# Performance work log

Measured on AMD Instinct MI355X. Metric: run time of the kernel, lower is better.

The kernel has to match this reference:

```python
import jax, jax.numpy as jnp
import numpy as np
from jax import lax

B, H, W = 4096, 8, 8
DICT, SE, E, NZ = 64, 8, 256, 1024
C1, C2 = 64, 128
EPS = 1e-4


def setup_inputs() -> dict:
    key = jax.random.key(0)
    ks = jax.random.split(key, 32)
    d = {}
    d['s'] = jax.random.randint(ks[0], (B, H, W), 0, DICT)
    d['s_prime'] = jax.random.randint(ks[1], (B, H, W), 0, DICT)
    d['w_embed'] = jax.random.normal(ks[2], (DICT, SE), dtype=jnp.float32)
    i = 3
    for p in ('p1', 'p2', 'p3'):
        d[p + '_w1'] = jax.random.normal(ks[i], (C1, SE, 3, 3), dtype=jnp.float32) * 0.1; i += 1
        d[p + '_b1'] = jax.random.normal(ks[i], (C1,), dtype=jnp.float32) * 0.1; i += 1
        d[p + '_w2'] = jax.random.normal(ks[i], (C2, C1, 3, 3), dtype=jnp.float32) * 0.05; i += 1
        d[p + '_b2'] = jax.random.normal(ks[i], (C2,), dtype=jnp.float32) * 0.05; i += 1
        d[p + '_lw'] = jax.random.normal(ks[i], (E, C2 * H * W), dtype=jnp.float32) * 0.02; i += 1
        d[p + '_lb'] = jax.random.normal(ks[i], (E,), dtype=jnp.float32) * 0.02; i += 1
    d['z_vectors'] = jax.random.normal(ks[i], (NZ, E), dtype=jnp.float32)
    d['scale'] = jnp.ones((1,), dtype=jnp.float32)
    return d


def _conv(x, w, b):
    # x: [B,C,H,W], w: [O,I,3,3], padding=1 == SAME for k=3
    y = lax.conv_general_dilated(x, w, (1, 1), 'SAME',
                                 dimension_numbers=('NCHW', 'OIHW', 'NCHW'))
    return y + b[None, :, None, None]


def _phi(x, w1, b1, w2, b2, lw, lb):
    # run_modules(..., last_activation=True): relu after every conv
    x = jax.nn.relu(_conv(x, w1, b1))
    x = jax.nn.relu(_conv(x, w2, b2))
    x = x.reshape(x.shape[0], -1)  # [B, C2*H*W]
    return x @ lw.T + lb  # [B, E]


def _normalized(m, eps):
    return m / (jnp.sqrt(jnp.sum(m * m, axis=1, keepdims=True)) + eps)


def reference(s, s_prime, w_embed,
              p1_w1, p1_b1, p1_w2, p1_b2, p1_lw, p1_lb,
              p2_w1, p2_b1, p2_w2, p2_b2, p2_lw, p2_lb,
              p3_w1, p3_b1, p3_w2, p3_b2, p3_lw, p3_lb,
              z_vectors, scale):
    # nn.Embedding(max_norm=1): renorm rows with norm > 1 to unit norm
    wn = jnp.sqrt(jnp.sum(w_embed * w_embed, axis=1, keepdims=True))
    w = w_embed * jnp.minimum(1.0, 1.0 / jnp.maximum(wn, 1e-7))
    s_embed = jnp.transpose(w[s], (0, 3, 1, 2))        # [B,SE,H,W]
    sp_embed = jnp.transpose(w[s_prime], (0, 3, 1, 2))  # embed_conv is None -> identity

    s_int = _phi(s_embed, p1_w1, p1_b1, p1_w2, p1_b2, p1_lw, p1_lb)            # phi1
    diff_int = _phi(sp_embed - s_embed, p2_w1, p2_b1, p2_w2, p2_b2, p2_lw, p2_lb)  # phi2
    sp_out = _normalized(_phi(sp_embed, p3_w1, p3_b1, p3_w2, p3_b2, p3_lw, p3_lb), EPS)  # phi3

    # quantize: cdist (p=2) against codebook, argmax (farthest, as in source), gather
    x2 = jnp.sum(diff_int * diff_int, axis=1, keepdims=True)      # [B,1]
    z2 = jnp.sum(z_vectors * z_vectors, axis=1)[None, :]          # [1,NZ]
    dist = jnp.sqrt(jnp.maximum(x2 + z2 - 2.0 * (diff_int @ z_vectors.T), 0.0))  # [B,NZ]
    z_inds = jnp.argmax(dist, axis=1)                              # [B]
    z_matrix = z_vectors[z_inds]                                   # [B,E]

    s_out = _normalized(s_int + z_matrix, EPS)                     # fc (fc_sizes=None)
    gram = s_out @ sp_out.T                                        # [B,B]
    return jnp.exp(scale) * gram
```

## Files before the change

### kernel.cpp

```cpp
#include <hip/hip_runtime.h>
#include <hip/hip_bf16.h>
#include <math.h>

#define NB 4096
#define SE 8
#define ND 64
#define C1 64
#define C2 128
#define NE 256
#define NZ 1024
#define CHUNK 2048
#define KACT 8192
#define KSPLIT 8

#define W1M_N (3*12*64*8)
#define W2M_N (3*18*128*32)
#define ZT_N  (256*1024)
#define PREP_TOTAL (W1M_N + W2M_N + ZT_N)
#define LW_N (NE*KACT)

typedef __attribute__((ext_vector_type(8))) short bf16x8;
typedef __attribute__((ext_vector_type(4))) float f32x4;
typedef __attribute__((ext_vector_type(8))) unsigned short u16x8;
typedef __attribute__((ext_vector_type(4))) unsigned short u16x4;

static __device__ __forceinline__ unsigned short f2bf(float v) {
  __hip_bfloat16 h = __float2bfloat16(v);
  return __builtin_bit_cast(unsigned short, h);
}
static __device__ __forceinline__ float bf2f(unsigned short u) {
  return __bfloat162float(__builtin_bit_cast(__hip_bfloat16, u));
}

__global__ __launch_bounds__(256) void prep_kernel(
    const float* __restrict__ w1_0, const float* __restrict__ w1_1, const float* __restrict__ w1_2,
    const float* __restrict__ w2_0, const float* __restrict__ w2_1, const float* __restrict__ w2_2,
    const float* __restrict__ z,
    unsigned short* __restrict__ w1mh, unsigned short* __restrict__ w1ml,
    unsigned short* __restrict__ w2mh, unsigned short* __restrict__ w2ml,
    float* __restrict__ zT)
{
  int idx = blockIdx.x * 256 + threadIdx.x;
  if (idx < W1M_N) {
    int p = idx / 6144; int r = idx - p*6144;
    int j = r >> 9; int rem = r & 511; int o = rem >> 3; int c = rem & 7;
    const float* w1 = (p == 0) ? w1_0 : (p == 1) ? w1_1 : w1_2;
    float v = (j < 9) ? w1[o*72 + c*9 + j] : 0.f;
    unsigned short h = f2bf(v);
    w1mh[idx] = h;
    w1ml[idx] = f2bf(v - bf2f(h));
  } else if (idx < W1M_N + W2M_N) {
    int r0 = idx - W1M_N;
    int p = r0 / (128*576); int r = r0 - p*(128*576);
    int o = r / 576; int rem = r - o*576; int j = rem >> 6; int c = rem & 63;
    const float* w2 = (p == 0) ? w2_0 : (p == 1) ? w2_1 : w2_2;
    float v = w2[o*576 + c*9 + j];
    unsigned short h = f2bf(v);
    const int d = p*(128*576) + ((j << 1) + (c >> 5))*4096 + o*32 + (c & 31);
    w2mh[d] = h;
    w2ml[d] = f2bf(v - bf2f(h));
  } else if (idx < PREP_TOTAL) {
    int r = idx - (W1M_N + W2M_N);
    int e = r >> 10, n = r & 1023;
    zT[r] = z[n*256 + e];
  }
}

__global__ __launch_bounds__(256) void prep_lw_kernel(
    const float* __restrict__ lw, unsigned short* __restrict__ lwh,
    unsigned short* __restrict__ lwl, int do_lo)
{
  int idx = blockIdx.x * 256 + threadIdx.x;
  float v = lw[idx];
  unsigned short h = f2bf(v);
  lwh[idx] = h;
  if (do_lo) lwl[idx] = f2bf(v - bf2f(h));
}

template<int PASSES>
__global__ __launch_bounds__(256, 4) void conv_phi_kernel(
    const int* __restrict__ s, const int* __restrict__ sp,
    const float* __restrict__ w_embed,
    const unsigned short* __restrict__ w1mh, const unsigned short* __restrict__ w1ml,
    const float* __restrict__ b1,
    const unsigned short* __restrict__ w2mh, const unsigned short* __restrict__ w2ml,
    const float* __restrict__ b2,
    unsigned short* __restrict__ acth, unsigned short* __restrict__ actl,
    int mode, int b_start)
{
  __shared__ float wtab[ND][SE+1];
  __shared__ int sidx[64];
  __shared__ int spidx[64];
  __shared__ __align__(16) unsigned short xph[960];
  __shared__ __align__(16) unsigned short xpl[960];
  __shared__ __align__(16) unsigned short c1h[7680];
  __shared__ __align__(16) unsigned short c1l[7680];

  const int tid = threadIdx.x;
  const int b = b_start + blockIdx.x;

  {
    int4 z4 = {0,0,0,0};
    for (int t = tid; t < 120; t += 256) { ((int4*)xph)[t] = z4; ((int4*)xpl)[t] = z4; }
    for (int t = tid; t < 960; t += 256) { ((int4*)c1h)[t] = z4; ((int4*)c1l)[t] = z4; }
  }

  if (tid < 64) {
    sidx[tid] = s[b*64 + tid];
    float v[SE]; float ss = 0.f;
    #pragma unroll
    for (int c = 0; c < SE; ++c) { v[c] = w_embed[tid*SE + c]; ss += v[c]*v[c]; }
    float nrm = sqrtf(ss);
    float sc = fminf(1.f, 1.f / fmaxf(nrm, 1e-7f));
    #pragma unroll
    for (int c = 0; c < SE; ++c) wtab[tid][c] = v[c] * sc;
  } else if (tid < 128) {
    spidx[tid - 64] = sp[b*64 + tid - 64];
  }
  __syncthreads();

  if (tid < 64) {
    const int y = tid >> 3, x = tid & 7;
    const float* r0 = wtab[sidx[tid]];
    const float* r1 = wtab[spidx[tid]];
    u16x8 hv, lv;
    #pragma unroll
    for (int c = 0; c < SE; ++c) {
      float e0 = r0[c], e1 = r1[c];
      float v = (mode == 0) ? e0 : (mode == 1) ? (e1 - e0) : e1;
      unsigned short h = f2bf(v);
      hv[c] = h;
      lv[c] = f2bf(v - bf2f(h));
    }
    const int lin = (y + 1)*12 + (x + 1);
    *(u16x8*)(xph + lin*8) = hv;
    *(u16x8*)(xpl + lin*8) = lv;
  }
  __syncthreads();

  {
    const int lane = tid & 63, wid = tid >> 6;
    const int ph = wid;
    const int l15 = lane & 15, lk4 = lane >> 4;

    f32x4 a1[4];
    #pragma unroll
    for (int fm = 0; fm < 4; ++fm) a1[fm] = (f32x4){0.f,0.f,0.f,0.f};

    #pragma unroll
    for (int kk = 0; kk < 3; ++kk) {
      const int j = (kk << 2) + lk4;
      const int jc = (j > 8) ? 8 : j;
      const int dy = jc / 3, dx = jc - 3*(jc/3);
      bf16x8 Wh[4], Wl[4];
      #pragma unroll
      for (int fm = 0; fm < 4; ++fm) {
        const int o = (fm << 4) + l15;
        Wh[fm] = *(const bf16x8*)(w1mh + (j << 9) + (o << 3));
        Wl[fm] = *(const bf16x8*)(w1ml + (j << 9) + (o << 3));
      }
      const int p = (ph << 4) + l15;
      const int lin = ((p >> 3) + dy)*12 + (p & 7) + dx;
      const bf16x8 Xh = *(const bf16x8*)(xph + (lin << 3));
      const bf16x8 Xl = *(const bf16x8*)(xpl + (lin << 3));
      __builtin_amdgcn_s_setprio(1);
      #pragma unroll
      for (int fm = 0; fm < 4; ++fm) {
        a1[fm] = __builtin_amdgcn_mfma_f32_16x16x32_bf16(Wh[fm], Xh, a1[fm], 0, 0, 0);
        a1[fm] = __builtin_amdgcn_mfma_f32_16x16x32_bf16(Wl[fm], Xh, a1[fm], 0, 0, 0);
        a1[fm] = __builtin_amdgcn_mfma_f32_16x16x32_bf16(Wh[fm], Xl, a1[fm], 0, 0, 0);
      }
      __builtin_amdgcn_s_setprio(0);
    }

    const int p = (ph << 4) + l15;
    const int lin = ((p >> 3) + 1)*12 + (p & 7) + 1;
    #pragma unroll
    for (int fm = 0; fm < 4; ++fm) {
      const int obase = (fm << 4) + (lk4 << 2);
      const float4 bv = *(const float4*)(b1 + obase);
      const int idx2 = (obase >> 3)*960 + lin*8 + (obase & 7);
      u16x4 hv, lv;
      {
        float v0 = fmaxf(a1[fm][0] + bv.x, 0.f);
        float v1 = fmaxf(a1[fm][1] + bv.y, 0.f);
        float v2 = fmaxf(a1[fm][2] + bv.z, 0.f);
        float v3 = fmaxf(a1[fm][3] + bv.w, 0.f);
        hv[0] = f2bf(v0); hv[1] = f2bf(v1); hv[2] = f2bf(v2); hv[3] = f2bf(v3);
        lv[0] = f2bf(v0 - bf2f(hv[0])); lv[1] = f2bf(v1 - bf2f(hv[1]));
        lv[2] = f2bf(v2 - bf2f(hv[2])); lv[3] = f2bf(v3 - bf2f(hv[3]));
      }
      *(u16x4*)(c1h + idx2) = hv;
      *(u16x4*)(c1l + idx2) = lv;
    }
  }
  __syncthreads();

  {
    const int lane = tid & 63, wid = tid >> 6;
    const int ob = wid << 5;
    const int l15 = lane & 15, lk4 = lane >> 4;
    const int y0b = l15 >> 3, x0 = l15 & 7;

    f32x4 acc[4][2];
    #pragma unroll
    for (int mf = 0; mf < 4; ++mf)
      #pragma unroll
      for (int nf = 0; nf < 2; ++nf) acc[mf][nf] = (f32x4){0.f,0.f,0.f,0.f};

    #pragma unroll
    for (int j = 0; j < 9; ++j) {
      const int dy = j / 3, dx = j - 3*(j/3);
      #pragma unroll
      for (int h2 = 0; h2 < 2; ++h2) {
        const int sbase = ((j << 1) + h2) << 12;
        bf16x8 Bh[2], Bl[2];
        #pragma unroll
        for (int nf = 0; nf < 2; ++nf) {
          const int orow = ob + (nf << 4) + l15;
          const int a = sbase + orow*32 + (lk4 << 3);
          Bh[nf] = *(const bf16x8*)(w2mh + a);
          if (PASSES == 3) Bl[nf] = *(const bf16x8*)(w2ml + a);
        }
        const int cbk = (h2 << 2) + lk4;
        bf16x8 Ah[4], Al[4];
        #pragma unroll
        for (int mf = 0; mf < 4; ++mf) {
          const int lin = ((mf << 1) + y0b + dy)*12 + x0 + dx;
          const int a = cbk*960 + lin*8;
          Ah[mf] = *(const bf16x8*)(c1h + a);
          Al[mf] = *(const bf16x8*)(c1l + a);
        }
        __builtin_amdgcn_s_setprio(1);
        #pragma unroll
        for (int mf = 0; mf < 4; ++mf) {
          #pragma unroll
          for (int nf = 0; nf < 2; ++nf) {
            acc[mf][nf] = __builtin_amdgcn_mfma_f32_16x16x32_bf16(Ah[mf], Bh[nf], acc[mf][nf], 0, 0, 0);
            acc[mf][nf] = __builtin_amdgcn_mfma_f32_16x16x32_bf16(Al[mf], Bh[nf], acc[mf][nf], 0, 0, 0);
            if (PASSES == 3)
              acc[mf][nf] = __builtin_amdgcn_mfma_f32_16x16x32_bf16(Ah[mf], Bl[nf], acc[mf][nf], 0, 0, 0);
          }
        }
        __builtin_amdgcn_s_setprio(0);
      }
    }

    const size_t rowbase = (size_t)blockIdx.x * 8192;
    #pragma unroll
    for (int nf = 0; nf < 2; ++nf) {
      const int col = ob + (nf << 4) + l15;
      const float bv = b2[col];
      #pragma unroll
      for (int mf = 0; mf < 4; ++mf) {
        const int p0 = mf*16 + lk4*4;
        u16x4 hv, lv;
        #pragma unroll
        for (int r2 = 0; r2 < 4; ++r2) {
          float v = fmaxf(acc[mf][nf][r2] + bv, 0.f);
          unsigned short hq = f2bf(v);
          hv[r2] = hq;
          lv[r2] = f2bf(v - bf2f(hq));
        }
        *(u16x4*)(acth + rowbase + col*64 + p0) = hv;
        if (PASSES == 3)
          *(u16x4*)(actl + rowbase + col*64 + p0) = lv;
      }
    }
  }
}

template<int PASSES>
__global__ __launch_bounds__(256) void gemm_lds_tn(
    const unsigned short* __restrict__ Ahp, const unsigned short* __restrict__ Alp,
    const unsigned short* __restrict__ Bhp, const unsigned short* __restrict__ Blp,
    int K, float* __restrict__ Cdirect, float* __restrict__ Cpart,
    const float* __restrict__ bias, const float* __restrict__ scale_ptr)
{
  constexpr int NOP = (PASSES == 3) ? 2 : 1;
  __shared__ __align__(16) unsigned short As[NOP][128*64];
  __shared__ __align__(16) unsigned short Bs[NOP][64*64];

  const int tid = threadIdx.x;
  const int lane = tid & 63, wid = tid >> 6;
  const int wm = wid >> 1, wn = wid & 1;
  const int l15 = lane & 15, lk4 = lane >> 4;
  const int M = gridDim.x << 7, N = gridDim.y << 6;
  const int KC = K / gridDim.z;
  const int bm = blockIdx.x << 7, bn = blockIdx.y << 6;
  const int kbase = blockIdx.z * KC;
  const int NT = KC >> 6;

  const int sr = tid >> 3;
  const int sc8 = (tid & 7) * 8;

  const unsigned short* gA[NOP];
  const unsigned short* gB[NOP];
  gA[0] = Ahp; gB[0] = Bhp;
  if (PASSES == 3) { gA[1] = Alp; gB[1] = Blp; }

  u16x8 ra[NOP][4], rb[NOP][2];

  f32x4 acc[4][2];
  #pragma unroll
  for (int fm = 0; fm < 4; ++fm)
    #pragma unroll
    for (int nf = 0; nf < 2; ++nf) acc[fm][nf] = (f32x4){0.f,0.f,0.f,0.f};

  {
    const int k0 = kbase + sc8;
    #pragma unroll
    for (int p = 0; p < NOP; ++p) {
      #pragma unroll
      for (int i = 0; i < 4; ++i)
        ra[p][i] = *(const u16x8*)(gA[p] + (size_t)(bm + sr + i*32) * K + k0);
      #pragma unroll
      for (int i = 0; i < 2; ++i)
        rb[p][i] = *(const u16x8*)(gB[p] + (size_t)(bn + sr + i*32) * K + k0);
    }
  }

  for (int t = 0; t < NT; ++t) {
    __syncthreads();
    #pragma unroll
    for (int p = 0; p < NOP; ++p) {
      #pragma unroll
      for (int i = 0; i < 4; ++i) {
        const int r = sr + i*32;
        *(u16x8*)(&As[p][r*64 + (sc8 ^ ((r & 7) << 3))]) = ra[p][i];
      }
      #pragma unroll
      for (int i = 0; i < 2; ++i) {
        const int r = sr + i*32;
        *(u16x8*)(&Bs[p][r*64 + (sc8 ^ ((r & 7) << 3))]) = rb[p][i];
      }
    }
    __syncthreads();
    if (t + 1 < NT) {
      const int k0 = kbase + ((t + 1) << 6) + sc8;
      #pragma unroll
      for (int p = 0; p < NOP; ++p) {
        #pragma unroll
        for (int i = 0; i < 4; ++i)
          ra[p][i] = *(const u16x8*)(gA[p] + (size_t)(bm + sr + i*32) * K + k0);
        #pragma unroll
        for (int i = 0; i < 2; ++i)
          rb[p][i] = *(const u16x8*)(gB[p] + (size_t)(bn + sr + i*32) * K + k0);
      }
    }
    #pragma unroll
    for (int ks = 0; ks < 2; ++ks) {
      const int kb = ks*32 + lk4*8;
      bf16x8 af[NOP][4], bf[NOP][2];
      #pragma unroll
      for (int p = 0; p < NOP; ++p) {
        #pragma unroll
        for (int fm = 0; fm < 4; ++fm) {
          const int r = wm*64 + fm*16 + l15;
          af[p][fm] = *(const bf16x8*)(&As[p][r*64 + (kb ^ ((r & 7) << 3))]);
        }
        #pragma unroll
        for (int nf = 0; nf < 2; ++nf) {
          const int r = wn*32 + nf*16 + l15;
          bf[p][nf] = *(const bf16x8*)(&Bs[p][r*64 + (kb ^ ((r & 7) << 3))]);
        }
      }
      #pragma unroll
      for (int fm = 0; fm < 4; ++fm) {
        #pragma unroll
        for (int nf = 0; nf < 2; ++nf) {
          acc[fm][nf] = __builtin_amdgcn_mfma_f32_16x16x32_bf16(af[0][fm], bf[0][nf], acc[fm][nf], 0, 0, 0);
          if (PASSES == 3) {
            acc[fm][nf] = __builtin_amdgcn_mfma_f32_16x16x32_bf16(af[0][fm], bf[1][nf], acc[fm][nf], 0, 0, 0);
            acc[fm][nf] = __builtin_amdgcn_mfma_f32_16x16x32_bf16(af[1][fm], bf[0][nf], acc[fm][nf], 0, 0, 0);
          }
        }
      }
    }
  }

  if (Cpart) {
    float* base = Cpart + (size_t)blockIdx.z * ((size_t)M * N);
    #pragma unroll
    for (int fm = 0; fm < 4; ++fm) {
      #pragma unroll
      for (int nf = 0; nf < 2; ++nf) {
        const int row0 = bm + wm*64 + fm*16 + lk4*4;
        const int col  = bn + wn*32 + nf*16 + l15;
        #pragma unroll
        for (int r2 = 0; r2 < 4; ++r2)
          base[(size_t)(row0 + r2) * N + col] = acc[fm][nf][r2];
      }
    }
  } else {
    float alpha = scale_ptr ? expf(scale_ptr[0]) : 1.f;
    #pragma unroll
    for (int fm = 0; fm < 4; ++fm) {
      #pragma unroll
      for (int nf = 0; nf < 2; ++nf) {
        const int row0 = bm + wm*64 + fm*16 + lk4*4;
        const int col  = bn + wn*32 + nf*16 + l15;
        const float bv = bias ? bias[col] : 0.f;
        #pragma unroll
        for (int r2 = 0; r2 < 4; ++r2)
          Cdirect[(size_t)(row0 + r2) * N + col] = alpha * acc[fm][nf][r2] + bv;
      }
    }
  }
}

__global__ __launch_bounds__(256) void reduce_bias_kernel(
    const float* __restrict__ part, const float* __restrict__ bias, float* __restrict__ out)
{
  const int idx = blockIdx.x * 256 + threadIdx.x;
  float a = bias[idx & (NE-1)];
  #pragma unroll
  for (int q = 0; q < KSPLIT; ++q) a += part[(size_t)q * (CHUNK*NE) + idx];
  out[idx] = a;
}

__global__ __launch_bounds__(256) void quant_kernel(
    const float* __restrict__ diff, const float* __restrict__ zT, int* __restrict__ z_ind)
{
  __shared__ __align__(16) float d[8][NE];
  __shared__ float wv[8][4];
  __shared__ int wni[8][4];
  const int tid = threadIdx.x;
  const int b0 = blockIdx.x * 8;
  for (int j = tid; j < 8*NE; j += 256) (&d[0][0])[j] = diff[(size_t)b0*NE + j];
  __syncthreads();

  float zz[4] = {0.f, 0.f, 0.f, 0.f};
  float dot[8][4] = {};
  for (int e = 0; e < NE; e += 4) {
    float4 dd[8];
    #pragma unroll
    for (int r = 0; r < 8; ++r) dd[r] = *(const float4*)(&d[r][e]);
    #pragma unroll
    for (int u = 0; u < 4; ++u) {
      const float* zr = zT + (size_t)(e + u) * NZ + tid;
      float z0 = zr[0], z1 = zr[256], z2 = zr[512], z3 = zr[768];
      zz[0] = fmaf(z0, z0, zz[0]); zz[1] = fmaf(z1, z1, zz[1]);
      zz[2] = fmaf(z2, z2, zz[2]); zz[3] = fmaf(z3, z3, zz[3]);
      #pragma unroll
      for (int r = 0; r < 8; ++r) {
        const float de = (u == 0) ? dd[r].x : (u == 1) ? dd[r].y : (u == 2) ? dd[r].z : dd[r].w;
        dot[r][0] = fmaf(z0, de, dot[r][0]);
        dot[r][1] = fmaf(z1, de, dot[r][1]);
        dot[r][2] = fmaf(z2, de, dot[r][2]);
        dot[r][3] = fmaf(z3, de, dot[r][3]);
      }
    }
  }

  const int lane = tid & 63, wid = tid >> 6;
  #pragma unroll
  for (int r = 0; r < 8; ++r) {
    float best = zz[0] - 2.f*dot[r][0]; int bi = tid;
    float v1 = zz[1] - 2.f*dot[r][1]; if (v1 > best) { best = v1; bi = tid + 256; }
    float v2 = zz[2] - 2.f*dot[r][2]; if (v2 > best) { best = v2; bi = tid + 512; }
    float v3 = zz[3] - 2.f*dot[r][3]; if (v3 > best) { best = v3; bi = tid + 768; }
    for (int m = 1; m < 64; m <<= 1) {
      float ov = __shfl_xor(best, m, 64);
      int   oi = __shfl_xor(bi, m, 64);
      if (ov > best || (ov == best && oi < bi)) { best = ov; bi = oi; }
    }
    if (lane == 0) { wv[r][wid] = best; wni[r][wid] = bi; }
  }
  __syncthreads();
  if (tid < 8) {
    float best = wv[tid][0]; int bi = wni[tid][0];
    #pragma unroll
    for (int w = 1; w < 4; ++w) {
      float v = wv[tid][w]; int n = wni[tid][w];
      if (v > best || (v == best && n < bi)) { best = v; bi = n; }
    }
    z_ind[b0 + tid] = bi;
  }
}

__global__ __launch_bounds__(256) void norm_to_bf16_kernel(
    const float* __restrict__ v, unsigned short* __restrict__ ob)
{
  const int row = blockIdx.x*4 + (threadIdx.x >> 6);
  const int lane = threadIdx.x & 63;
  float4 x = ((const float4*)v)[(size_t)row*64 + lane];
  float ss = x.x*x.x + x.y*x.y + x.z*x.z + x.w*x.w;
  #pragma unroll
  for (int m = 1; m < 64; m <<= 1) ss += __shfl_xor(ss, m, 64);
  float sc = 1.f / (sqrtf(ss) + 1e-4f);
  u16x4 o;
  o[0] = f2bf(x.x*sc); o[1] = f2bf(x.y*sc); o[2] = f2bf(x.z*sc); o[3] = f2bf(x.w*sc);
  *(u16x4*)(ob + (size_t)row*NE + lane*4) = o;
}

__global__ __launch_bounds__(256) void build_sout_kernel(
    const float* __restrict__ s_int, const float* __restrict__ z,
    const int* __restrict__ z_ind, unsigned short* __restrict__ ob)
{
  const int row = blockIdx.x*4 + (threadIdx.x >> 6);
  const int lane = threadIdx.x & 63;
  const int zi = z_ind[row];
  float4 a = *((const float4*)s_int + (size_t)row*64 + lane);
  float4 c = *((const float4*)z + (size_t)zi*64 + lane);
  float4 x = {a.x + c.x, a.y + c.y, a.z + c.z, a.w + c.w};
  float ss = x.x*x.x + x.y*x.y + x.z*x.z + x.w*x.w;
  #pragma unroll
  for (int m = 1; m < 64; m <<= 1) ss += __shfl_xor(ss, m, 64);
  float sc = 1.f / (sqrtf(ss) + 1e-4f);
  u16x4 o;
  o[0] = f2bf(x.x*sc); o[1] = f2bf(x.y*sc); o[2] = f2bf(x.z*sc); o[3] = f2bf(x.w*sc);
  *(u16x4*)(ob + (size_t)row*NE + lane*4) = o;
}

extern "C" void kernel_launch(void* const* d_in, const int* in_sizes, int n_in,
                              void* d_out, int out_size, void* d_ws, size_t ws_size,
                              hipStream_t stream)
{
  const int* s  = (const int*)d_in[0];
  const int* sp = (const int*)d_in[1];
  const float* w_embed = (const float*)d_in[2];
  const float* z = (const float*)d_in[21];
  const float* scale = (const float*)d_in[22];
  float* out = (float*)d_out;

  size_t off = 0;
  auto allocB = [&](size_t bytes) -> void* {
    void* p = (void*)((char*)d_ws + off);
    off += ((bytes + 255) & ~(size_t)255);
    return p;
  };
  unsigned short* w1mh  = (unsigned short*)allocB((size_t)W1M_N * 2);
  unsigned short* w1ml  = (unsigned short*)allocB((size_t)W1M_N * 2);
  unsigned short* w2mh  = (unsigned short*)allocB((size_t)W2M_N * 2);
  unsigned short* w2ml  = (unsigned short*)allocB((size_t)W2M_N * 2);
  float* zT             = (float*)allocB(ZT_N * 4);
  unsigned short* lwh   = (unsigned short*)allocB((size_t)LW_N * 2);
  unsigned short* lwl   = (unsigned short*)allocB((size_t)LW_N * 2);
  float* s_int          = (float*)allocB((size_t)NB * NE * 4);
  float* diff_int       = (float*)allocB((size_t)NB * NE * 4);
  float* sp_out         = (float*)allocB((size_t)NB * NE * 4);
  unsigned short* soutb = (unsigned short*)allocB((size_t)NB * NE * 2);
  unsigned short* spoutb= (unsigned short*)allocB((size_t)NB * NE * 2);
  int*   z_ind          = (int*)allocB(NB * 4);
  float* part           = (float*)allocB((size_t)CHUNK * NE * KSPLIT * 4);

  unsigned short* acth = (unsigned short*)d_out;
  unsigned short* actl = acth + (size_t)CHUNK * KACT;

  prep_kernel<<<PREP_TOTAL/256, 256, 0, stream>>>(
      (const float*)d_in[3],  (const float*)d_in[9],  (const float*)d_in[15],
      (const float*)d_in[5],  (const float*)d_in[11], (const float*)d_in[17],
      z, w1mh, w1ml, w2mh, w2ml, zT);

  for (int phi = 0; phi < 3; ++phi) {
    const float* b1 = (const float*)d_in[4 + phi*6];
    const float* b2 = (const float*)d_in[6 + phi*6];
    const float* lw = (const float*)d_in[7 + phi*6];
    const float* lb = (const float*)d_in[8 + phi*6];
    float* outvec = (phi == 0) ? s_int : (phi == 1) ? diff_int : sp_out;

    prep_lw_kernel<<<LW_N/256, 256, 0, stream>>>(lw, lwh, lwl, phi == 1);

    for (int b0 = 0; b0 < NB; b0 += CHUNK) {
      if (phi == 1)
        conv_phi_kernel<3><<<CHUNK, 256, 0, stream>>>(
            s, sp, w_embed, w1mh + phi*6144, w1ml + phi*6144, b1,
            w2mh + phi*(128*576), w2ml + phi*(128*576), b2,
            acth, actl, phi, b0);
      else
        conv_phi_kernel<2><<<CHUNK, 256, 0, stream>>>(
            s, sp, w_embed, w1mh + phi*6144, w1ml + phi*6144, b1,
            w2mh + phi*(128*576), w2ml + phi*(128*576), b2,
            acth, actl, phi, b0);
      dim3 g(CHUNK/128, NE/64, KSPLIT);
      if (phi == 1)
        gemm_lds_tn<3><<<g, 256, 0, stream>>>(acth, actl, lwh, lwl,
            KACT, nullptr, part, nullptr, nullptr);
      else
        gemm_lds_tn<1><<<g, 256, 0, stream>>>(acth, nullptr, lwh, nullptr,
            KACT, nullptr, part, nullptr, nullptr);
      reduce_bias_kernel<<<(CHUNK*NE)/256, 256, 0, stream>>>(part, lb, outvec + (size_t)b0*NE);
    }
  }

  norm_to_bf16_kernel<<<NB/4, 256, 0, stream>>>(sp_out, spoutb);
  quant_kernel<<<NB/8, 256, 0, stream>>>(diff_int, zT, z_ind);
  build_sout_kernel<<<NB/4, 256, 0, stream>>>(s_int, z, z_ind, soutb);

  dim3 gg(NB/128, NB/64, 1);
  gemm_lds_tn<1><<<gg, 256, 0, stream>>>(soutb, nullptr, spoutb, nullptr,
      NE, out, nullptr, nullptr, scale);
}
```

Baseline: 531.4 us.

## Switch conv2 to 32x32x16 MFMA tiles and precompute normalized embedding table

Measured after the change: 561.3 us. 5.6% more time.

```diff
diff --git a/kernel.cpp b/kernel.cpp
--- a/kernel.cpp
+++ b/kernel.cpp
@@ -14,13 +14,15 @@
 #define KSPLIT 8
 
 #define W1M_N (3*12*64*8)
-#define W2M_N (3*18*128*32)
+#define W2M_N (3*36*128*16)
 #define ZT_N  (256*1024)
 #define PREP_TOTAL (W1M_N + W2M_N + ZT_N)
+#define PREP_TOTAL2 (PREP_TOTAL + 512)
 #define LW_N (NE*KACT)
 
 typedef __attribute__((ext_vector_type(8))) short bf16x8;
 typedef __attribute__((ext_vector_type(4))) float f32x4;
+typedef __attribute__((ext_vector_type(16))) float f32x16;
 typedef __attribute__((ext_vector_type(8))) unsigned short u16x8;
 typedef __attribute__((ext_vector_type(4))) unsigned short u16x4;
 
@@ -35,10 +37,10 @@
 __global__ __launch_bounds__(256) void prep_kernel(
     const float* __restrict__ w1_0, const float* __restrict__ w1_1, const float* __restrict__ w1_2,
     const float* __restrict__ w2_0, const float* __restrict__ w2_1, const float* __restrict__ w2_2,
-    const float* __restrict__ z,
+    const float* __restrict__ z, const float* __restrict__ w_embed,
     unsigned short* __restrict__ w1mh, unsigned short* __restrict__ w1ml,
     unsigned short* __restrict__ w2mh, unsigned short* __restrict__ w2ml,
-    float* __restrict__ zT)
+    float* __restrict__ zT, float* __restrict__ wnorm)
 {
   int idx = blockIdx.x * 256 + threadIdx.x;
   if (idx < W1M_N) {
@@ -52,17 +54,28 @@
   } else if (idx < W1M_N + W2M_N) {
     int r0 = idx - W1M_N;
     int p = r0 / (128*576); int r = r0 - p*(128*576);
-    int o = r / 576; int rem = r - o*576; int j = rem >> 6; int c = rem & 63;
+    int slice = r >> 11; int rem = r & 2047;
+    int och = rem >> 4; int k = rem & 15;
+    int j = slice >> 2, q = slice & 3;
+    int c = (q << 4) + k;
     const float* w2 = (p == 0) ? w2_0 : (p == 1) ? w2_1 : w2_2;
-    float v = w2[o*576 + c*9 + j];
+    float v = w2[och*576 + c*9 + j];
     unsigned short h = f2bf(v);
-    const int d = p*(128*576) + ((j << 1) + (c >> 5))*4096 + o*32 + (c & 31);
-    w2mh[d] = h;
-    w2ml[d] = f2bf(v - bf2f(h));
+    w2mh[r0] = h;
+    w2ml[r0] = f2bf(v - bf2f(h));
   } else if (idx < PREP_TOTAL) {
     int r = idx - (W1M_N + W2M_N);
     int e = r >> 10, n = r & 1023;
     zT[r] = z[n*256 + e];
+  } else if (idx < PREP_TOTAL2) {
+    int t = idx - PREP_TOTAL;
+    int o = t >> 3, c = t & 7;
+    float ss = 0.f;
+    #pragma unroll
+    for (int e = 0; e < 8; ++e) { float u = w_embed[o*8 + e]; ss += u*u; }
+    float nrm = sqrtf(ss);
+    float sc = fminf(1.f, 1.f / fmaxf(nrm, 1e-7f));
+    wnorm[o*8 + c] = w_embed[o*8 + c] * sc;
   }
 }
 
@@ -80,7 +93,7 @@
 template<int PASSES>
 __global__ __launch_bounds__(256, 4) void conv_phi_kernel(
     const int* __restrict__ s, const int* __restrict__ sp,
-    const float* __restrict__ w_embed,
+    const float* __restrict__ wnorm,
     const unsigned short* __restrict__ w1mh, const unsigned short* __restrict__ w1ml,
     const float* __restrict__ b1,
     const unsigned short* __restrict__ w2mh, const unsigned short* __restrict__ w2ml,
@@ -88,9 +101,6 @@
     unsigned short* __restrict__ acth, unsigned short* __restrict__ actl,
     int mode, int b_start)
 {
-  __shared__ float wtab[ND][SE+1];
-  __shared__ int sidx[64];
-  __shared__ int spidx[64];
   __shared__ __align__(16) unsigned short xph[960];
   __shared__ __align__(16) unsigned short xpl[960];
   __shared__ __align__(16) unsigned short c1h[7680];
@@ -104,35 +114,26 @@
     for (int t = tid; t < 120; t += 256) { ((int4*)xph)[t] = z4; ((int4*)xpl)[t] = z4; }
     for (int t = tid; t < 960; t += 256) { ((int4*)c1h)[t] = z4; ((int4*)c1l)[t] = z4; }
   }
+  __syncthreads();
 
   if (tid < 64) {
-    sidx[tid] = s[b*64 + tid];
-    float v[SE]; float ss = 0.f;
-    #pragma unroll
-    for (int c = 0; c < SE; ++c) { v[c] = w_embed[tid*SE + c]; ss += v[c]*v[c]; }
-    float nrm = sqrtf(ss);
-    float sc = fminf(1.f, 1.f / fmaxf(nrm, 1e-7f));
-    #pragma unroll
-    for (int c = 0; c < SE; ++c) wtab[tid][c] = v[c] * sc;
-  } else if (tid < 128) {
-    spidx[tid - 64] = sp[b*64 + tid - 64];
-  }
-  __syncthreads();
-
-  if (tid < 64) {
-    const int y = tid >> 3, x = tid & 7;
-    const float* r0 = wtab[sidx[tid]];
-    const float* r1 = wtab[spidx[tid]];
+    const int si  = s[b*64 + tid];
+    const int spi = sp[b*64 + tid];
+    const float4 a0 = *(const float4*)(wnorm + si*8);
+    const float4 a1v = *(const float4*)(wnorm + si*8 + 4);
+    const float4 c0 = *(const float4*)(wnorm + spi*8);
+    const float4 c1v = *(const float4*)(wnorm + spi*8 + 4);
+    float e0[8] = {a0.x,a0.y,a0.z,a0.w, a1v.x,a1v.y,a1v.z,a1v.w};
+    float e1[8] = {c0.x,c0.y,c0.z,c0.w, c1v.x,c1v.y,c1v.z,c1v.w};
     u16x8 hv, lv;
     #pragma unroll
     for (int c = 0; c < SE; ++c) {
-      float e0 = r0[c], e1 = r1[c];
-      float v = (mode == 0) ? e0 : (mode == 1) ? (e1 - e0) : e1;
+      float v = (mode == 0) ? e0[c] : (mode == 1) ? (e1[c] - e0[c]) : e1[c];
       unsigned short h = f2bf(v);
       hv[c] = h;
       lv[c] = f2bf(v - bf2f(h));
     }
-    const int lin = (y + 1)*12 + (x + 1);
+    const int lin = ((tid >> 3) + 1)*12 + (tid & 7) + 1;
     *(u16x8*)(xph + lin*8) = hv;
     *(u16x8*)(xpl + lin*8) = lv;
   }
@@ -198,49 +199,44 @@
 
   {
     const int lane = tid & 63, wid = tid >> 6;
-    const int ob = wid << 5;
-    const int l15 = lane & 15, lk4 = lane >> 4;
-    const int y0b = l15 >> 3, x0 = l15 & 7;
-
-    f32x4 acc[4][2];
-    #pragma unroll
-    for (int mf = 0; mf < 4; ++mf)
-      #pragma unroll
-      for (int nf = 0; nf < 2; ++nf) acc[mf][nf] = (f32x4){0.f,0.f,0.f,0.f};
+    const int mt = wid >> 1;
+    const int np = wid & 1;
+    const int l31 = lane & 31, lh = lane >> 5;
+    const int p = (mt << 5) + l31;
+    const int py = p >> 3, px = p & 7;
+
+    f32x16 acc[2];
+    #pragma unroll
+    for (int nt = 0; nt < 2; ++nt)
+      #pragma unroll
+      for (int e = 0; e < 16; ++e) acc[nt][e] = 0.f;
 
     #pragma unroll
     for (int j = 0; j < 9; ++j) {
       const int dy = j / 3, dx = j - 3*(j/3);
-      #pragma unroll
-      for (int h2 = 0; h2 < 2; ++h2) {
-        const int sbase = ((j << 1) + h2) << 12;
+      const int lin = (py + dy)*12 + px + dx;
+      #pragma unroll
+      for (int q = 0; q < 4; ++q) {
+        const int slice = (j << 2) + q;
+        const int cb = (q << 1) + lh;
+        const int aofs = cb*960 + (lin << 3);
+        const bf16x8 Ah = *(const bf16x8*)(c1h + aofs);
+        const bf16x8 Al = *(const bf16x8*)(c1l + aofs);
         bf16x8 Bh[2], Bl[2];
         #pragma unroll
-        for (int nf = 0; nf < 2; ++nf) {
-          const int orow = ob + (nf << 4) + l15;
-          const int a = sbase + orow*32 + (lk4 << 3);
-          Bh[nf] = *(const bf16x8*)(w2mh + a);
-          if (PASSES == 3) Bl[nf] = *(const bf16x8*)(w2ml + a);
-        }
-        const int cbk = (h2 << 2) + lk4;
-        bf16x8 Ah[4], Al[4];
-        #pragma unroll
-        for (int mf = 0; mf < 4; ++mf) {
-          const int lin = ((mf << 1) + y0b + dy)*12 + x0 + dx;
-          const int a = cbk*960 + lin*8;
-          Ah[mf] = *(const bf16x8*)(c1h + a);
-          Al[mf] = *(const bf16x8*)(c1l + a);
+        for (int nt = 0; nt < 2; ++nt) {
+          const int och = (np << 6) + (nt << 5) + l31;
+          const int bofs = (slice << 11) + (och << 4) + (lh << 3);
+          Bh[nt] = *(const bf16x8*)(w2mh + bofs);
+          if (PASSES == 3) Bl[nt] = *(const bf16x8*)(w2ml + bofs);
         }
         __builtin_amdgcn_s_setprio(1);
         #pragma unroll
-        for (int mf = 0; mf < 4; ++mf) {
-          #pragma unroll
-          for (int nf = 0; nf < 2; ++nf) {
-            acc[mf][nf] = __builtin_amdgcn_mfma_f32_16x16x32_bf16(Ah[mf], Bh[nf], acc[mf][nf], 0, 0, 0);
-            acc[mf][nf] = __builtin_amdgcn_mfma_f32_16x16x32_bf16(Al[mf], Bh[nf], acc[mf][nf], 0, 0, 0);
-            if (PASSES == 3)
-              acc[mf][nf] = __builtin_amdgcn_mfma_f32_16x16x32_bf16(Ah[mf], Bl[nf], acc[mf][nf], 0, 0, 0);
-          }
+        for (int nt = 0; nt < 2; ++nt) {
+          acc[nt] = __builtin_amdgcn_mfma_f32_32x32x16_bf16(Ah, Bh[nt], acc[nt], 0, 0, 0);
+          acc[nt] = __builtin_amdgcn_mfma_f32_32x32x16_bf16(Al, Bh[nt], acc[nt], 0, 0, 0);
+          if (PASSES == 3)
+            acc[nt] = __builtin_amdgcn_mfma_f32_32x32x16_bf16(Ah, Bl[nt], acc[nt], 0, 0, 0);
         }
         __builtin_amdgcn_s_setprio(0);
       }
@@ -248,23 +244,23 @@
 
     const size_t rowbase = (size_t)blockIdx.x * 8192;
     #pragma unroll
-    for (int nf = 0; nf < 2; ++nf) {
-      const int col = ob + (nf << 4) + l15;
+    for (int nt = 0; nt < 2; ++nt) {
+      const int col = (np << 6) + (nt << 5) + l31;
       const float bv = b2[col];
       #pragma unroll
-      for (int mf = 0; mf < 4; ++mf) {
-        const int p0 = mf*16 + lk4*4;
+      for (int rq = 0; rq < 4; ++rq) {
+        const int prow = (mt << 5) + (rq << 3) + (lh << 2);
         u16x4 hv, lv;
         #pragma unroll
-        for (int r2 = 0; r2 < 4; ++r2) {
-          float v = fmaxf(acc[mf][nf][r2] + bv, 0.f);
+        for (int rr = 0; rr < 4; ++rr) {
+          float v = fmaxf(acc[nt][(rq << 2) + rr] + bv, 0.f);
           unsigned short hq = f2bf(v);
-          hv[r2] = hq;
-          lv[r2] = f2bf(v - bf2f(hq));
+          hv[rr] = hq;
+          lv[rr] = f2bf(v - bf2f(hq));
         }
-        *(u16x4*)(acth + rowbase + col*64 + p0) = hv;
+        *(u16x4*)(acth + rowbase + col*64 + prow) = hv;
         if (PASSES == 3)
-          *(u16x4*)(actl + rowbase + col*64 + p0) = lv;
+          *(u16x4*)(actl + rowbase + col*64 + prow) = lv;
       }
     }
   }
@@ -535,6 +531,7 @@
   unsigned short* w2mh  = (unsigned short*)allocB((size_t)W2M_N * 2);
   unsigned short* w2ml  = (unsigned short*)allocB((size_t)W2M_N * 2);
   float* zT             = (float*)allocB(ZT_N * 4);
+  float* wnorm          = (float*)allocB(64 * 8 * 4);
   unsigned short* lwh   = (unsigned short*)allocB((size_t)LW_N * 2);
   unsigned short* lwl   = (unsigned short*)allocB((size_t)LW_N * 2);
   float* s_int          = (float*)allocB((size_t)NB * NE * 4);
@@ -548,10 +545,10 @@
   unsigned short* acth = (unsigned short*)d_out;
   unsigned short* actl = acth + (size_t)CHUNK * KACT;
 
-  prep_kernel<<<PREP_TOTAL/256, 256, 0, stream>>>(
+  prep_kernel<<<PREP_TOTAL2/256, 256, 0, stream>>>(
       (const float*)d_in[3],  (const float*)d_in[9],  (const float*)d_in[15],
       (const float*)d_in[5],  (const float*)d_in[11], (const float*)d_in[17],
-      z, w1mh, w1ml, w2mh, w2ml, zT);
+      z, w_embed, w1mh, w1ml, w2mh, w2ml, zT, wnorm);
 
   for (int phi = 0; phi < 3; ++phi) {
     const float* b1 = (const float*)d_in[4 + phi*6];
@@ -565,12 +562,12 @@
     for (int b0 = 0; b0 < NB; b0 += CHUNK) {
       if (phi == 1)
         conv_phi_kernel<3><<<CHUNK, 256, 0, stream>>>(
-            s, sp, w_embed, w1mh + phi*6144, w1ml + phi*6144, b1,
+            s, sp, wnorm, w1mh + phi*6144, w1ml + phi*6144, b1,
             w2mh + phi*(128*576), w2ml + phi*(128*576), b2,
             acth, actl, phi, b0);
       else
         conv_phi_kernel<2><<<CHUNK, 256, 0, stream>>>(
-            s, sp, w_embed, w1mh + phi*6144, w1ml + phi*6144, b1,
+            s, sp, wnorm, w1mh + phi*6144, w1ml + phi*6144, b1,
             w2mh + phi*(128*576), w2ml + phi*(128*576), b2,
             acth, actl, phi, b0);
       dim3 g(CHUNK/128, NE/64, KSPLIT);
```

## Precompute normalized embedding table and retile conv2 warp layout to 2x4 fragments

Applied to the files above, without the earlier changes.

Result: slower. 621.6 us (+17.0%).

```diff
diff --git a/kernel.cpp b/kernel.cpp
--- a/kernel.cpp
+++ b/kernel.cpp
@@ -17,6 +17,7 @@
 #define W2M_N (3*18*128*32)
 #define ZT_N  (256*1024)
 #define PREP_TOTAL (W1M_N + W2M_N + ZT_N)
+#define PREP_TOTAL2 (PREP_TOTAL + 512)
 #define LW_N (NE*KACT)
 
 typedef __attribute__((ext_vector_type(8))) short bf16x8;
@@ -35,10 +36,10 @@
 __global__ __launch_bounds__(256) void prep_kernel(
     const float* __restrict__ w1_0, const float* __restrict__ w1_1, const float* __restrict__ w1_2,
     const float* __restrict__ w2_0, const float* __restrict__ w2_1, const float* __restrict__ w2_2,
-    const float* __restrict__ z,
+    const float* __restrict__ z, const float* __restrict__ w_embed,
     unsigned short* __restrict__ w1mh, unsigned short* __restrict__ w1ml,
     unsigned short* __restrict__ w2mh, unsigned short* __restrict__ w2ml,
-    float* __restrict__ zT)
+    float* __restrict__ zT, float* __restrict__ wnorm)
 {
   int idx = blockIdx.x * 256 + threadIdx.x;
   if (idx < W1M_N) {
@@ -63,6 +64,15 @@
     int r = idx - (W1M_N + W2M_N);
     int e = r >> 10, n = r & 1023;
     zT[r] = z[n*256 + e];
+  } else if (idx < PREP_TOTAL2) {
+    int t = idx - PREP_TOTAL;
+    int o = t >> 3, c = t & 7;
+    float ss = 0.f;
+    #pragma unroll
+    for (int e = 0; e < 8; ++e) { float u = w_embed[o*8 + e]; ss += u*u; }
+    float nrm = sqrtf(ss);
+    float sc = fminf(1.f, 1.f / fmaxf(nrm, 1e-7f));
+    wnorm[o*8 + c] = w_embed[o*8 + c] * sc;
   }
 }
 
@@ -80,7 +90,7 @@
 template<int PASSES>
 __global__ __launch_bounds__(256, 4) void conv_phi_kernel(
     const int* __restrict__ s, const int* __restrict__ sp,
-    const float* __restrict__ w_embed,
+    const float* __restrict__ wnorm,
     const unsigned short* __restrict__ w1mh, const unsigned short* __restrict__ w1ml,
     const float* __restrict__ b1,
     const unsigned short* __restrict__ w2mh, const unsigned short* __restrict__ w2ml,
@@ -88,9 +98,6 @@
     unsigned short* __restrict__ acth, unsigned short* __restrict__ actl,
     int mode, int b_start)
 {
-  __shared__ float wtab[ND][SE+1];
-  __shared__ int sidx[64];
-  __shared__ int spidx[64];
   __shared__ __align__(16) unsigned short xph[960];
   __shared__ __align__(16) unsigned short xpl[960];
   __shared__ __align__(16) unsigned short c1h[7680];
@@ -104,35 +111,26 @@
     for (int t = tid; t < 120; t += 256) { ((int4*)xph)[t] = z4; ((int4*)xpl)[t] = z4; }
     for (int t = tid; t < 960; t += 256) { ((int4*)c1h)[t] = z4; ((int4*)c1l)[t] = z4; }
   }
+  __syncthreads();
 
   if (tid < 64) {
-    sidx[tid] = s[b*64 + tid];
-    float v[SE]; float ss = 0.f;
-    #pragma unroll
-    for (int c = 0; c < SE; ++c) { v[c] = w_embed[tid*SE + c]; ss += v[c]*v[c]; }
-    float nrm = sqrtf(ss);
-    float sc = fminf(1.f, 1.f / fmaxf(nrm, 1e-7f));
-    #pragma unroll
-    for (int c = 0; c < SE; ++c) wtab[tid][c] = v[c] * sc;
-  } else if (tid < 128) {
-    spidx[tid - 64] = sp[b*64 + tid - 64];
-  }
-  __syncthreads();
-
-  if (tid < 64) {
-    const int y = tid >> 3, x = tid & 7;
-    const float* r0 = wtab[sidx[tid]];
-    const float* r1 = wtab[spidx[tid]];
+    const int si  = s[b*64 + tid];
+    const int spi = sp[b*64 + tid];
+    const float4 a0 = *(const float4*)(wnorm + si*8);
+    const float4 a1v = *(const float4*)(wnorm + si*8 + 4);
+    const float4 c0 = *(const float4*)(wnorm + spi*8);
+    const float4 c1v = *(const float4*)(wnorm + spi*8 + 4);
+    float e0[8] = {a0.x,a0.y,a0.z,a0.w, a1v.x,a1v.y,a1v.z,a1v.w};
+    float e1[8] = {c0.x,c0.y,c0.z,c0.w, c1v.x,c1v.y,c1v.z,c1v.w};
     u16x8 hv, lv;
     #pragma unroll
     for (int c = 0; c < SE; ++c) {
-      float e0 = r0[c], e1 = r1[c];
-      float v = (mode == 0) ? e0 : (mode == 1) ? (e1 - e0) : e1;
+      float v = (mode == 0) ? e0[c] : (mode == 1) ? (e1[c] - e0[c]) : e1[c];
       unsigned short h = f2bf(v);
       hv[c] = h;
       lv[c] = f2bf(v - bf2f(h));
     }
-    const int lin = (y + 1)*12 + (x + 1);
+    const int lin = ((tid >> 3) + 1)*12 + (tid & 7) + 1;
     *(u16x8*)(xph + lin*8) = hv;
     *(u16x8*)(xpl + lin*8) = lv;
   }
@@ -198,15 +196,15 @@
 
   {
     const int lane = tid & 63, wid = tid >> 6;
-    const int ob = wid << 5;
+    const int mh = wid >> 1;
+    const int oh = wid & 1;
     const int l15 = lane & 15, lk4 = lane >> 4;
-    const int y0b = l15 >> 3, x0 = l15 & 7;
-
-    f32x4 acc[4][2];
-    #pragma unroll
-    for (int mf = 0; mf < 4; ++mf)
-      #pragma unroll
-      for (int nf = 0; nf < 2; ++nf) acc[mf][nf] = (f32x4){0.f,0.f,0.f,0.f};
+
+    f32x4 acc[2][4];
+    #pragma unroll
+    for (int mf = 0; mf < 2; ++mf)
+      #pragma unroll
+      for (int nf = 0; nf < 4; ++nf) acc[mf][nf] = (f32x4){0.f,0.f,0.f,0.f};
 
     #pragma unroll
     for (int j = 0; j < 9; ++j) {
@@ -214,28 +212,29 @@
       #pragma unroll
       for (int h2 = 0; h2 < 2; ++h2) {
         const int sbase = ((j << 1) + h2) << 12;
-        bf16x8 Bh[2], Bl[2];
-        #pragma unroll
-        for (int nf = 0; nf < 2; ++nf) {
-          const int orow = ob + (nf << 4) + l15;
+        bf16x8 Bh[4], Bl[4];
+        #pragma unroll
+        for (int nf = 0; nf < 4; ++nf) {
+          const int orow = (oh << 6) + (nf << 4) + l15;
           const int a = sbase + orow*32 + (lk4 << 3);
           Bh[nf] = *(const bf16x8*)(w2mh + a);
           if (PASSES == 3) Bl[nf] = *(const bf16x8*)(w2ml + a);
         }
         const int cbk = (h2 << 2) + lk4;
-        bf16x8 Ah[4], Al[4];
-        #pragma unroll
-        for (int mf = 0; mf < 4; ++mf) {
-          const int lin = ((mf << 1) + y0b + dy)*12 + x0 + dx;
-          const int a = cbk*960 + lin*8;
+        bf16x8 Ah[2], Al[2];
+        #pragma unroll
+        for (int mf = 0; mf < 2; ++mf) {
+          const int p = (mh << 5) + (mf << 4) + l15;
+          const int lin = ((p >> 3) + dy)*12 + (p & 7) + dx;
+          const int a = cbk*960 + (lin << 3);
           Ah[mf] = *(const bf16x8*)(c1h + a);
           Al[mf] = *(const bf16x8*)(c1l + a);
         }
         __builtin_amdgcn_s_setprio(1);
         #pragma unroll
-        for (int mf = 0; mf < 4; ++mf) {
+        for (int mf = 0; mf < 2; ++mf) {
           #pragma unroll
-          for (int nf = 0; nf < 2; ++nf) {
+          for (int nf = 0; nf < 4; ++nf) {
             acc[mf][nf] = __builtin_amdgcn_mfma_f32_16x16x32_bf16(Ah[mf], Bh[nf], acc[mf][nf], 0, 0, 0);
             acc[mf][nf] = __builtin_amdgcn_mfma_f32_16x16x32_bf16(Al[mf], Bh[nf], acc[mf][nf], 0, 0, 0);
             if (PASSES == 3)
@@ -248,12 +247,12 @@
 
     const size_t rowbase = (size_t)blockIdx.x * 8192;
     #pragma unroll
-    for (int nf = 0; nf < 2; ++nf) {
-      const int col = ob + (nf << 4) + l15;
+    for (int nf = 0; nf < 4; ++nf) {
+      const int col = (oh << 6) + (nf << 4) + l15;
       const float bv = b2[col];
       #pragma unroll
-      for (int mf = 0; mf < 4; ++mf) {
-        const int p0 = mf*16 + lk4*4;
+      for (int mf = 0; mf < 2; ++mf) {
+        const int p0 = (mh << 5) + (mf << 4) + lk4*4;
         u16x4 hv, lv;
         #pragma unroll
         for (int r2 = 0; r2 < 4; ++r2) {
@@ -535,6 +534,7 @@
   unsigned short* w2mh  = (unsigned short*)allocB((size_t)W2M_N * 2);
   unsigned short* w2ml  = (unsigned short*)allocB((size_t)W2M_N * 2);
   float* zT             = (float*)allocB(ZT_N * 4);
+  float* wnorm          = (float*)allocB(64 * 8 * 4);
   unsigned short* lwh   = (unsigned short*)allocB((size_t)LW_N * 2);
   unsigned short* lwl   = (unsigned short*)allocB((size_t)LW_N * 2);
   float* s_int          = (float*)allocB((size_t)NB * NE * 4);
@@ -548,10 +548,10 @@
   unsigned short* acth = (unsigned short*)d_out;
   unsigned short* actl = acth + (size_t)CHUNK * KACT;
 
-  prep_kernel<<<PREP_TOTAL/256, 256, 0, stream>>>(
+  prep_kernel<<<PREP_TOTAL2/256, 256, 0, stream>>>(
       (const float*)d_in[3],  (const float*)d_in[9],  (const float*)d_in[15],
       (const float*)d_in[5],  (const float*)d_in[11], (const float*)d_in[17],
-      z, w1mh, w1ml, w2mh, w2ml, zT);
+      z, w_embed, w1mh, w1ml, w2mh, w2ml, zT, wnorm);
 
   for (int phi = 0; phi < 3; ++phi) {
     const float* b1 = (const float*)d_in[4 + phi*6];
@@ -565,12 +565,12 @@
     for (int b0 = 0; b0 < NB; b0 += CHUNK) {
       if (phi == 1)
         conv_phi_kernel<3><<<CHUNK, 256, 0, stream>>>(
-            s, sp, w_embed, w1mh + phi*6144, w1ml + phi*6144, b1,
+            s, sp, wnorm, w1mh + phi*6144, w1ml + phi*6144, b1,
             w2mh + phi*(128*576), w2ml + phi*(128*576), b2,
             acth, actl, phi, b0);
       else
         conv_phi_kernel<2><<<CHUNK, 256, 0, stream>>>(
-            s, sp, w_embed, w1mh + phi*6144, w1ml + phi*6144, b1,
+            s, sp, wnorm, w1mh + phi*6144, w1ml + phi*6144, b1,
             w2mh + phi*(128*576), w2ml + phi*(128*576), b2,
             acth, actl, phi, b0);
       dim3 g(CHUNK/128, NE/64, KSPLIT);
```
